# Optimization experiments

Measured on AMD Instinct MI355X. Metric: run time of the kernel, lower is better.

Reference implementation:

```python
import jax, jax.numpy as jnp
import numpy as np

NUM_GRAPHS = 1024
N_NODES = 8388608

def setup_inputs() -> dict:
    key = jax.random.key(0)
    k1, k2, k3 = jax.random.split(key, 3)
    positions = jax.random.normal(k1, (N_NODES, 3), dtype=jnp.float32)
    q = jax.random.normal(k2, (N_NODES,), dtype=jnp.float32)
    batch = jnp.sort(jax.random.randint(k3, (N_NODES,), 0, NUM_GRAPHS, dtype=jnp.int64))
    return {"positions": positions, "q": q, "batch": batch}

def reference(positions, q, batch):
    # q: [N] -> [N,1]; remove global mean over all nodes (remove_mean=True)
    qc = q[:, None] - jnp.mean(q)
    # per-graph polarization: sum_i q_i * r_i  -> [NUM_GRAPHS, 3]
    pol = jax.ops.segment_sum(qc * positions, batch, num_segments=NUM_GRAPHS)
    return pol
```

## Files before the change

### kernel.cpp

```cpp
#include <hip/hip_runtime.h>


#define N_NODES     8388608
#define NUM_GRAPHS  1024
#define BLK         256
#define TILE_NODES  1024
#define NT          (N_NODES / TILE_NODES)
#define G4          (TILE_NODES / 4)

#define IBASE_OFF   16
#define SPLIT_OFF   (IBASE_OFF + NT)
#define REC_OFF     (SPLIT_OFF + 4 * NT)
#define REC_STRIDE  16
#define EXTRA_OFF   (REC_OFF + NT * REC_STRIDE)
#define WS_FLOATS   (EXTRA_OFF + NUM_GRAPHS * 6)

__global__ __launch_bounds__(BLK) void split_kernel(const int* __restrict__ batch,
                                                    float* __restrict__ ws) {
    int b = blockIdx.x * BLK + threadIdx.x;
    if (b >= NT) return;
    if (b < 2048) {
        float* extra = ws + EXTRA_OFF;
        extra[b * 3 + 0] = 0.f; extra[b * 3 + 1] = 0.f; extra[b * 3 + 2] = 0.f;
    }
    const int s = b * TILE_NODES;
    const int e = s + TILE_NODES;
    int i0 = batch[s];
    int i1 = batch[e - 1];
    int split = e;
    if (i1 != i0) {
        int lo = s + 1, hi = e - 1;
        while (lo < hi) {
            int mid = (lo + hi) >> 1;
            if (batch[mid] > i0) hi = mid; else lo = mid + 1;
        }
        split = lo;
    }
    ((int4*)(ws + SPLIT_OFF))[b] = make_int4(i0, i1, split, 0);
    ((int*)(ws + IBASE_OFF))[b] = i0;
}

__global__ __launch_bounds__(BLK) void pol_main(const float4* __restrict__ p4,
                                                const float4* __restrict__ q4,
                                                const int*    __restrict__ batch,
                                                float* __restrict__ ws) {
    const int lane = threadIdx.x & 63;
    const int w    = blockIdx.x * 4 + (threadIdx.x >> 6);
    float* extra = ws + EXTRA_OFF;

    const int4 si = ((const int4*)(ws + SPLIT_OFF))[w];
    const int i0 = si.x, i1 = si.y, split = si.z;
    const bool general = (i1 > i0 + 1);

    const int vi0 = w * G4;
    float4 Q[4], P0[4], P1[4], P2[4];
    #pragma unroll
    for (int j = 0; j < 4; ++j) {
        int vi = vi0 + j * 64 + lane;
        Q[j]  = q4[vi];
        P0[j] = p4[3 * vi + 0];
        P1[j] = p4[3 * vi + 1];
        P2[j] = p4[3 * vi + 2];
    }

    float qsum = 0.f;
    float aqx = 0, aqy = 0, aqz = 0, arx = 0, ary = 0, arz = 0;
    float bqx = 0, bqy = 0, bqz = 0, brx = 0, bry = 0, brz = 0;

    if (!general) {
        #pragma unroll
        for (int j = 0; j < 4; ++j) {
            int n0 = (vi0 + j * 64 + lane) * 4;
            float qs[4] = {Q[j].x, Q[j].y, Q[j].z, Q[j].w};
            float px[4] = {P0[j].x, P0[j].w, P1[j].z, P2[j].y};
            float py[4] = {P0[j].y, P1[j].x, P1[j].w, P2[j].z};
            float pz[4] = {P0[j].z, P1[j].y, P2[j].x, P2[j].w};
            qsum += (qs[0] + qs[1]) + (qs[2] + qs[3]);
            #pragma unroll
            for (int k = 0; k < 4; ++k) {
                if (n0 + k < split) {
                    aqx = fmaf(qs[k], px[k], aqx); aqy = fmaf(qs[k], py[k], aqy);
                    aqz = fmaf(qs[k], pz[k], aqz);
                    arx += px[k]; ary += py[k]; arz += pz[k];
                } else {
                    bqx = fmaf(qs[k], px[k], bqx); bqy = fmaf(qs[k], py[k], bqy);
                    bqz = fmaf(qs[k], pz[k], bqz);
                    brx += px[k]; bry += py[k]; brz += pz[k];
                }
            }
        }
    } else {
        #pragma unroll
        for (int j = 0; j < 4; ++j) {
            int n0 = (vi0 + j * 64 + lane) * 4;
            float qs[4] = {Q[j].x, Q[j].y, Q[j].z, Q[j].w};
            float px[4] = {P0[j].x, P0[j].w, P1[j].z, P2[j].y};
            float py[4] = {P0[j].y, P1[j].x, P1[j].w, P2[j].z};
            float pz[4] = {P0[j].z, P1[j].y, P2[j].x, P2[j].w};
            for (int k = 0; k < 4; ++k) {
                int id = batch[n0 + k];
                qsum += qs[k];
                atomicAdd(&extra[id * 6 + 0], qs[k] * px[k]);
                atomicAdd(&extra[id * 6 + 1], qs[k] * py[k]);
                atomicAdd(&extra[id * 6 + 2], qs[k] * pz[k]);
                atomicAdd(&extra[id * 6 + 3], px[k]);
                atomicAdd(&extra[id * 6 + 4], py[k]);
                atomicAdd(&extra[id * 6 + 5], pz[k]);
            }
        }
    }

    #pragma unroll
    for (int off = 32; off > 0; off >>= 1) {
        qsum += __shfl_down(qsum, off, 64);
        aqx += __shfl_down(aqx, off, 64); aqy += __shfl_down(aqy, off, 64);
        aqz += __shfl_down(aqz, off, 64); arx += __shfl_down(arx, off, 64);
        ary += __shfl_down(ary, off, 64); arz += __shfl_down(arz, off, 64);
    }
    if (i1 != i0 && !general) {
        #pragma unroll
        for (int off = 32; off > 0; off >>= 1) {
            bqx += __shfl_down(bqx, off, 64); bqy += __shfl_down(bqy, off, 64);
            bqz += __shfl_down(bqz, off, 64); brx += __shfl_down(brx, off, 64);
            bry += __shfl_down(bry, off, 64); brz += __shfl_down(brz, off, 64);
        }
    }

    if (lane == 0) {
        float* rec = ws + REC_OFF + (size_t)w * REC_STRIDE;
        rec[0] = qsum;
        rec[4] = aqx; rec[5] = aqy; rec[6] = aqz;
        rec[7] = arx; rec[8] = ary; rec[9] = arz;
        rec[10] = bqx; rec[11] = bqy; rec[12] = bqz;
        rec[13] = brx; rec[14] = bry; rec[15] = brz;
    }
}

__global__ __launch_bounds__(1024) void finalize_kernel(const float* __restrict__ ws,
                                                        float* __restrict__ out) {
    __shared__ float sm[16];
    __shared__ float smean;
    const int t = threadIdx.x;

    float s = 0.f;
    for (int i = t; i < NT; i += 1024) s += ws[REC_OFF + (size_t)i * REC_STRIDE];
    #pragma unroll
    for (int off = 32; off > 0; off >>= 1) s += __shfl_down(s, off, 64);
    if ((t & 63) == 0) sm[t >> 6] = s;
    __syncthreads();
    if (t == 0) {
        float tot = 0.f;
        #pragma unroll
        for (int i = 0; i < 16; ++i) tot += sm[i];
        smean = tot * (1.0f / (float)N_NODES);
    }
    __syncthreads();
    const float mean = smean;

    const int g = t;
    const int* ibase = (const int*)(ws + IBASE_OFF);
    const int4* sp4  = (const int4*)(ws + SPLIT_OFF);
    const float* extra = ws + EXTRA_OFF;

    float qx = extra[g * 6 + 0], qy = extra[g * 6 + 1], qz = extra[g * 6 + 2];
    float rx = extra[g * 6 + 3], ry = extra[g * 6 + 4], rz = extra[g * 6 + 5];

    int lo = 0, hi = NT - 1, B = -1;
    while (lo <= hi) {
        int mid = (lo + hi) >> 1;
        if (ibase[mid] <= g) { B = mid; lo = mid + 1; } else hi = mid - 1;
    }
    for (int b = B; b >= 0; --b) {
        int4 sb = sp4[b];
        if (sb.y < g) break;
        const float* r = ws + REC_OFF + (size_t)b * REC_STRIDE;
        if (sb.x == g) {
            qx += r[4]; qy += r[5]; qz += r[6];
            rx += r[7]; ry += r[8]; rz += r[9];
        }
        if (sb.y == g && sb.y != sb.x) {
            qx += r[10]; qy += r[11]; qz += r[12];
            rx += r[13]; ry += r[14]; rz += r[15];
        }
    }
    out[g * 3 + 0] = fmaf(-mean, rx, qx);
    out[g * 3 + 1] = fmaf(-mean, ry, qy);
    out[g * 3 + 2] = fmaf(-mean, rz, qz);
}


__global__ void sum_q_kernel(const float* __restrict__ q, float* __restrict__ ws, int n4) {
    int tid = blockIdx.x * blockDim.x + threadIdx.x;
    int stride = gridDim.x * blockDim.x;
    const float4* q4 = (const float4*)q;
    float s = 0.f;
    for (int i = tid; i < n4; i += stride) {
        float4 v = q4[i];
        s += (v.x + v.y) + (v.z + v.w);
    }
    for (int off = 32; off > 0; off >>= 1) s += __shfl_down(s, off, 64);
    __shared__ float smem[4];
    int lane = threadIdx.x & 63, wave = threadIdx.x >> 6;
    if (lane == 0) smem[wave] = s;
    __syncthreads();
    if (threadIdx.x == 0) atomicAdd(ws, (smem[0] + smem[1]) + (smem[2] + smem[3]));
}

__global__ void pol_atomic_kernel(const float* __restrict__ pos,
                                  const float* __restrict__ q,
                                  const int*   __restrict__ batch,
                                  const float* __restrict__ ws,
                                  float* __restrict__ out, int n) {
    const float mean = ws[0] * (1.0f / (float)N_NODES);
    int tid = blockIdx.x * blockDim.x + threadIdx.x;
    int stride = gridDim.x * blockDim.x;
    int n4 = n >> 2;
    const float4* q4 = (const float4*)q;
    const int4*   b4 = (const int4*)batch;
    const float4* p4 = (const float4*)pos;

    for (int i = tid; i < n4; i += stride) {
        float4 qv = q4[i];
        int4   bv = b4[i];
        float4 p0 = p4[3 * i + 0];
        float4 p1 = p4[3 * i + 1];
        float4 p2 = p4[3 * i + 2];
        float qs[4] = {qv.x - mean, qv.y - mean, qv.z - mean, qv.w - mean};
        int  ids[4] = {bv.x, bv.y, bv.z, bv.w};
        float px[4] = {p0.x, p0.w, p1.z, p2.y};
        float py[4] = {p0.y, p1.x, p1.w, p2.z};
        float pz[4] = {p0.z, p1.y, p2.x, p2.w};
        int cur = ids[0];
        float sx = 0.f, sy = 0.f, sz = 0.f;
        #pragma unroll
        for (int j = 0; j < 4; ++j) {
            if (ids[j] != cur) {
                atomicAdd(&out[cur * 3 + 0], sx);
                atomicAdd(&out[cur * 3 + 1], sy);
                atomicAdd(&out[cur * 3 + 2], sz);
                sx = sy = sz = 0.f;
                cur = ids[j];
            }
            sx = fmaf(qs[j], px[j], sx);
            sy = fmaf(qs[j], py[j], sy);
            sz = fmaf(qs[j], pz[j], sz);
        }
        int first = __shfl(cur, 0, 64);
        bool uniform = __all(cur == first);
        if (uniform) {
            for (int off = 32; off > 0; off >>= 1) {
                sx += __shfl_down(sx, off, 64);
                sy += __shfl_down(sy, off, 64);
                sz += __shfl_down(sz, off, 64);
            }
            if ((threadIdx.x & 63) == 0) {
                atomicAdd(&out[cur * 3 + 0], sx);
                atomicAdd(&out[cur * 3 + 1], sy);
                atomicAdd(&out[cur * 3 + 2], sz);
            }
        } else {
            atomicAdd(&out[cur * 3 + 0], sx);
            atomicAdd(&out[cur * 3 + 1], sy);
            atomicAdd(&out[cur * 3 + 2], sz);
        }
    }
}

extern "C" void kernel_launch(void* const* d_in, const int* in_sizes, int n_in,
                              void* d_out, int out_size, void* d_ws, size_t ws_size,
                              hipStream_t stream) {
    const float* pos   = (const float*)d_in[0];
    const float* q     = (const float*)d_in[1];
    const int*   batch = (const int*)d_in[2];
    float* out = (float*)d_out;
    float* ws  = (float*)d_ws;
    int n = in_sizes[1];

    if (ws_size >= (size_t)WS_FLOATS * sizeof(float)) {
        split_kernel<<<NT / BLK, BLK, 0, stream>>>(batch, ws);
        pol_main<<<NT / 4, BLK, 0, stream>>>((const float4*)pos, (const float4*)q,
                                             batch, ws);
        finalize_kernel<<<1, 1024, 0, stream>>>(ws, out);
    } else {
        hipMemsetAsync(d_out, 0, (size_t)out_size * sizeof(float), stream);
        hipMemsetAsync(d_ws, 0, sizeof(float), stream);
        sum_q_kernel<<<4096, BLK, 0, stream>>>(q, ws, n >> 2);
        pol_atomic_kernel<<<8192, BLK, 0, stream>>>(pos, q, batch, ws, out, n);
    }
}
```

Baseline: 214.8 us.

## Make pol_main persistent with double-buffered tile loads across four tiles per wave

Halves the tile size and launches a fixed 4096 waves, each processing four strided tiles. Loads of the next tile are issued into a second register buffer before the current tile is reduced, so memory latency overlaps with compute. This adds register pressure and more per-tile records and split-kernel work, which finalize must now sweep, and it relies on NT being exactly four times WAVES_TOT.

Measured after the change: 232.9 us. 8.4% more time.

```diff
diff --git a/kernel.cpp b/kernel.cpp
--- a/kernel.cpp
+++ b/kernel.cpp
@@ -4,9 +4,11 @@
 #define N_NODES     8388608
 #define NUM_GRAPHS  1024
 #define BLK         256
-#define TILE_NODES  1024
+#define TILE_NODES  512
 #define NT          (N_NODES / TILE_NODES)
-#define G4          (TILE_NODES / 4)
+#define G4T         (TILE_NODES / 4)
+#define WAVES_TOT   4096
+#define TPW         (NT / WAVES_TOT)
 
 #define IBASE_OFF   16
 #define SPLIT_OFF   (IBASE_OFF + NT)
@@ -40,100 +42,116 @@
     ((int*)(ws + IBASE_OFF))[b] = i0;
 }
 
+struct Buf { float4 Q[2], P0[2], P1[2], P2[2]; };
+
 __global__ __launch_bounds__(BLK) void pol_main(const float4* __restrict__ p4,
                                                 const float4* __restrict__ q4,
                                                 const int*    __restrict__ batch,
                                                 float* __restrict__ ws) {
     const int lane = threadIdx.x & 63;
-    const int w    = blockIdx.x * 4 + (threadIdx.x >> 6);
+    const int W    = blockIdx.x * 4 + (threadIdx.x >> 6);
     float* extra = ws + EXTRA_OFF;
-
-    const int4 si = ((const int4*)(ws + SPLIT_OFF))[w];
-    const int i0 = si.x, i1 = si.y, split = si.z;
-    const bool general = (i1 > i0 + 1);
-
-    const int vi0 = w * G4;
-    float4 Q[4], P0[4], P1[4], P2[4];
-    #pragma unroll
-    for (int j = 0; j < 4; ++j) {
-        int vi = vi0 + j * 64 + lane;
-        Q[j]  = q4[vi];
-        P0[j] = p4[3 * vi + 0];
-        P1[j] = p4[3 * vi + 1];
-        P2[j] = p4[3 * vi + 2];
-    }
-
-    float qsum = 0.f;
-    float aqx = 0, aqy = 0, aqz = 0, arx = 0, ary = 0, arz = 0;
-    float bqx = 0, bqy = 0, bqz = 0, brx = 0, bry = 0, brz = 0;
-
-    if (!general) {
+    const int4* sp4 = (const int4*)(ws + SPLIT_OFF);
+
+    auto load_tile = [&](int T, Buf& B) {
+        int vi0 = T * G4T;
         #pragma unroll
-        for (int j = 0; j < 4; ++j) {
-            int n0 = (vi0 + j * 64 + lane) * 4;
-            float qs[4] = {Q[j].x, Q[j].y, Q[j].z, Q[j].w};
-            float px[4] = {P0[j].x, P0[j].w, P1[j].z, P2[j].y};
-            float py[4] = {P0[j].y, P1[j].x, P1[j].w, P2[j].z};
-            float pz[4] = {P0[j].z, P1[j].y, P2[j].x, P2[j].w};
-            qsum += (qs[0] + qs[1]) + (qs[2] + qs[3]);
+        for (int j = 0; j < 2; ++j) {
+            int vi = vi0 + j * 64 + lane;
+            B.Q[j]  = q4[vi];
+            B.P0[j] = p4[3 * vi + 0];
+            B.P1[j] = p4[3 * vi + 1];
+            B.P2[j] = p4[3 * vi + 2];
+        }
+    };
+
+    auto reduce_tile = [&](int T, int4 si, const Buf& Bf) {
+        const int i0 = si.x, i1 = si.y, split = si.z;
+        const bool general = (i1 > i0 + 1);
+        float qsum = 0.f;
+        float aqx = 0, aqy = 0, aqz = 0, arx = 0, ary = 0, arz = 0;
+        float bqx = 0, bqy = 0, bqz = 0, brx = 0, bry = 0, brz = 0;
+
+        if (!general) {
             #pragma unroll
-            for (int k = 0; k < 4; ++k) {
-                if (n0 + k < split) {
-                    aqx = fmaf(qs[k], px[k], aqx); aqy = fmaf(qs[k], py[k], aqy);
-                    aqz = fmaf(qs[k], pz[k], aqz);
-                    arx += px[k]; ary += py[k]; arz += pz[k];
-                } else {
-                    bqx = fmaf(qs[k], px[k], bqx); bqy = fmaf(qs[k], py[k], bqy);
-                    bqz = fmaf(qs[k], pz[k], bqz);
-                    brx += px[k]; bry += py[k]; brz += pz[k];
+            for (int j = 0; j < 2; ++j) {
+                int n0 = (T * G4T + j * 64 + lane) * 4;
+                float qs[4] = {Bf.Q[j].x, Bf.Q[j].y, Bf.Q[j].z, Bf.Q[j].w};
+                float px[4] = {Bf.P0[j].x, Bf.P0[j].w, Bf.P1[j].z, Bf.P2[j].y};
+                float py[4] = {Bf.P0[j].y, Bf.P1[j].x, Bf.P1[j].w, Bf.P2[j].z};
+                float pz[4] = {Bf.P0[j].z, Bf.P1[j].y, Bf.P2[j].x, Bf.P2[j].w};
+                qsum += (qs[0] + qs[1]) + (qs[2] + qs[3]);
+                #pragma unroll
+                for (int k = 0; k < 4; ++k) {
+                    if (n0 + k < split) {
+                        aqx = fmaf(qs[k], px[k], aqx); aqy = fmaf(qs[k], py[k], aqy);
+                        aqz = fmaf(qs[k], pz[k], aqz);
+                        arx += px[k]; ary += py[k]; arz += pz[k];
+                    } else {
+                        bqx = fmaf(qs[k], px[k], bqx); bqy = fmaf(qs[k], py[k], bqy);
+                        bqz = fmaf(qs[k], pz[k], bqz);
+                        brx += px[k]; bry += py[k]; brz += pz[k];
+                    }
                 }
             }
-        }
-    } else {
-        #pragma unroll
-        for (int j = 0; j < 4; ++j) {
-            int n0 = (vi0 + j * 64 + lane) * 4;
-            float qs[4] = {Q[j].x, Q[j].y, Q[j].z, Q[j].w};
-            float px[4] = {P0[j].x, P0[j].w, P1[j].z, P2[j].y};
-            float py[4] = {P0[j].y, P1[j].x, P1[j].w, P2[j].z};
-            float pz[4] = {P0[j].z, P1[j].y, P2[j].x, P2[j].w};
-            for (int k = 0; k < 4; ++k) {
-                int id = batch[n0 + k];
-                qsum += qs[k];
-                atomicAdd(&extra[id * 6 + 0], qs[k] * px[k]);
-                atomicAdd(&extra[id * 6 + 1], qs[k] * py[k]);
-                atomicAdd(&extra[id * 6 + 2], qs[k] * pz[k]);
-                atomicAdd(&extra[id * 6 + 3], px[k]);
-                atomicAdd(&extra[id * 6 + 4], py[k]);
-                atomicAdd(&extra[id * 6 + 5], pz[k]);
-            }
-        }
-    }
-
-    #pragma unroll
-    for (int off = 32; off > 0; off >>= 1) {
-        qsum += __shfl_down(qsum, off, 64);
-        aqx += __shfl_down(aqx, off, 64); aqy += __shfl_down(aqy, off, 64);
-        aqz += __shfl_down(aqz, off, 64); arx += __shfl_down(arx, off, 64);
-        ary += __shfl_down(ary, off, 64); arz += __shfl_down(arz, off, 64);
-    }
-    if (i1 != i0 && !general) {
+        } else {
+            #pragma unroll
+            for (int j = 0; j < 2; ++j) {
+                int n0 = (T * G4T + j * 64 + lane) * 4;
+                float qs[4] = {Bf.Q[j].x, Bf.Q[j].y, Bf.Q[j].z, Bf.Q[j].w};
+                float px[4] = {Bf.P0[j].x, Bf.P0[j].w, Bf.P1[j].z, Bf.P2[j].y};
+                float py[4] = {Bf.P0[j].y, Bf.P1[j].x, Bf.P1[j].w, Bf.P2[j].z};
+                float pz[4] = {Bf.P0[j].z, Bf.P1[j].y, Bf.P2[j].x, Bf.P2[j].w};
+                for (int k = 0; k < 4; ++k) {
+                    int id = batch[n0 + k];
+                    qsum += qs[k];
+                    atomicAdd(&extra[id * 6 + 0], qs[k] * px[k]);
+                    atomicAdd(&extra[id * 6 + 1], qs[k] * py[k]);
+                    atomicAdd(&extra[id * 6 + 2], qs[k] * pz[k]);
+                    atomicAdd(&extra[id * 6 + 3], px[k]);
+                    atomicAdd(&extra[id * 6 + 4], py[k]);
+                    atomicAdd(&extra[id * 6 + 5], pz[k]);
+                }
+            }
+        }
+
         #pragma unroll
         for (int off = 32; off > 0; off >>= 1) {
-            bqx += __shfl_down(bqx, off, 64); bqy += __shfl_down(bqy, off, 64);
-            bqz += __shfl_down(bqz, off, 64); brx += __shfl_down(brx, off, 64);
-            bry += __shfl_down(bry, off, 64); brz += __shfl_down(brz, off, 64);
-        }
-    }
-
-    if (lane == 0) {
-        float* rec = ws + REC_OFF + (size_t)w * REC_STRIDE;
-        rec[0] = qsum;
-        rec[4] = aqx; rec[5] = aqy; rec[6] = aqz;
-        rec[7] = arx; rec[8] = ary; rec[9] = arz;
-        rec[10] = bqx; rec[11] = bqy; rec[12] = bqz;
-        rec[13] = brx; rec[14] = bry; rec[15] = brz;
-    }
+            qsum += __shfl_down(qsum, off, 64);
+            aqx += __shfl_down(aqx, off, 64); aqy += __shfl_down(aqy, off, 64);
+            aqz += __shfl_down(aqz, off, 64); arx += __shfl_down(arx, off, 64);
+            ary += __shfl_down(ary, off, 64); arz += __shfl_down(arz, off, 64);
+        }
+        if (i1 != i0 && !general) {
+            #pragma unroll
+            for (int off = 32; off > 0; off >>= 1) {
+                bqx += __shfl_down(bqx, off, 64); bqy += __shfl_down(bqy, off, 64);
+                bqz += __shfl_down(bqz, off, 64); brx += __shfl_down(brx, off, 64);
+                bry += __shfl_down(bry, off, 64); brz += __shfl_down(brz, off, 64);
+            }
+        }
+        if (lane == 0) {
+            float* rec = ws + REC_OFF + (size_t)T * REC_STRIDE;
+            rec[0] = qsum;
+            rec[4] = aqx; rec[5] = aqy; rec[6] = aqz;
+            rec[7] = arx; rec[8] = ary; rec[9] = arz;
+            rec[10] = bqx; rec[11] = bqy; rec[12] = bqz;
+            rec[13] = brx; rec[14] = bry; rec[15] = brz;
+        }
+    };
+
+    const int T0 = W, T1 = W + WAVES_TOT, T2 = W + 2 * WAVES_TOT, T3 = W + 3 * WAVES_TOT;
+    const int4 s0 = sp4[T0], s1 = sp4[T1], s2 = sp4[T2], s3 = sp4[T3];
+
+    Buf A, B;
+    load_tile(T0, A);
+    load_tile(T1, B);
+    reduce_tile(T0, s0, A);
+    load_tile(T2, A);
+    reduce_tile(T1, s1, B);
+    load_tile(T3, B);
+    reduce_tile(T2, s2, A);
+    reduce_tile(T3, s3, B);
 }
 
 __global__ __launch_bounds__(1024) void finalize_kernel(const float* __restrict__ ws,
@@ -278,8 +296,8 @@
 
     if (ws_size >= (size_t)WS_FLOATS * sizeof(float)) {
         split_kernel<<<NT / BLK, BLK, 0, stream>>>(batch, ws);
-        pol_main<<<NT / 4, BLK, 0, stream>>>((const float4*)pos, (const float4*)q,
-                                             batch, ws);
+        pol_main<<<WAVES_TOT / 4, BLK, 0, stream>>>((const float4*)pos,
+                                                    (const float4*)q, batch, ws);
         finalize_kernel<<<1, 1024, 0, stream>>>(ws, out);
     } else {
         hipMemsetAsync(d_out, 0, (size_t)out_size * sizeof(float), stream);
```
